# Kernel optimization log

Hardware: AMD Instinct MI355X
Metric: run time of the kernel (lower is better)

Reference implementation:

```python
import jax, jax.numpy as jnp
import numpy as np

N_QUBITS = 13
N_LAYERS = 8
DIM = 2 ** N_QUBITS
CDT = jnp.complex64

_X = jnp.array([[0.0, 1.0], [1.0, 0.0]], dtype=CDT)
_Z = jnp.array([[1.0, 0.0], [0.0, -1.0]], dtype=CDT)
_I2 = jnp.eye(2, dtype=CDT)
_CNOT = jnp.array([[1, 0, 0, 0], [0, 1, 0, 0], [0, 0, 0, 1], [0, 0, 1, 0]], dtype=CDT)


def build_ops():
    """Hardware-efficient ansatz: per layer RX on all qubits, RZ on all qubits, CNOT chain."""
    ops = []
    p = 0
    for _ in range(N_LAYERS):
        for q in range(N_QUBITS):
            ops.append(('RX', (q,), p)); p += 1
        for q in range(N_QUBITS):
            ops.append(('RZ', (q,), p)); p += 1
        for q in range(N_QUBITS - 1):
            ops.append(('CNOT', (q, q + 1), None))
    return ops, p

OPS, N_PARAMS = build_ops()


def _rot(generator, theta):
    # U = cos(theta/2) I - i sin(theta/2) G
    h = theta * 0.5
    return jnp.cos(h).astype(CDT) * _I2 - 1j * jnp.sin(h).astype(CDT) * generator


def _apply_1q(state, U, q):
    st = state.reshape((2,) * N_QUBITS)
    st = jnp.tensordot(U, st, axes=([1], [q]))  # contracted axis moves to front
    return jnp.moveaxis(st, 0, q).reshape(-1)


def _apply_2q(state, U, q0, q1):
    st = state.reshape((2,) * N_QUBITS)
    st = jnp.tensordot(U.reshape(2, 2, 2, 2), st, axes=([2, 3], [q0, q1]))
    return jnp.moveaxis(st, (0, 1), (q0, q1)).reshape(-1)


def _run_circuit(params):
    state = jnp.zeros(DIM, dtype=CDT).at[0].set(1.0)
    for gate, qubits, pidx in OPS:
        if gate == 'RX':
            state = _apply_1q(state, _rot(_X, params[pidx]), qubits[0])
        elif gate == 'RZ':
            state = _apply_1q(state, _rot(_Z, params[pidx]), qubits[0])
        else:  # CNOT
            state = _apply_2q(state, _CNOT, qubits[0], qubits[1])
    return state


def setup_inputs() -> dict:
    key = jax.random.key(0)
    k1, k2 = jax.random.split(key)
    params = jax.random.normal(k1, (N_PARAMS,), dtype=jnp.float32)
    observable = jax.random.normal(k2, (DIM, DIM), dtype=jnp.float32)
    return {"params": params, "observable": observable}


def reference(params, observable) -> jnp.ndarray:
    psi = _run_circuit(params)                      # [2^n] complex64
    obs_psi = observable.astype(CDT) @ psi          # dense observable matvec
    loss = jnp.vdot(psi, obs_psi).real.astype(jnp.float32)  # <psi|O|psi>
    return loss
```

## Files before the change

kernel.cpp:

```cpp
#include <hip/hip_runtime.h>

#define DIM 8192
#define NLAYERS 8
#define SIMT 1024
#define QFB 2048
#define QFT 256
#define ROWS_PER_BLOCK 4

typedef float floatx4 __attribute__((ext_vector_type(4)));
typedef float f2 __attribute__((ext_vector_type(2)));

__device__ __forceinline__ int swz(int i) { return i ^ ((i >> 4) & 15); }

__global__ __launch_bounds__(SIMT) void sim_kernel(const float* __restrict__ params,
                                                   float* __restrict__ outR,
                                                   float* __restrict__ outM) {
    __shared__ f2 buf[2][DIM];
    const int t = threadIdx.x;

    f2 a[8];
#pragma unroll
    for (int l = 0; l < 8; ++l) a[l] = (f2){0.f, 0.f};
    if (t == 0) a[0] = (f2){1.f, 0.f};

    int pp = 0;

    for (int layer = 0; layer < NLAYERS; ++layer) {
        const float* __restrict__ prx = params + layer * 26;
        const float* __restrict__ prz = prx + 13;

        float cb[13], sb[13];
#pragma unroll
        for (int p = 0; p < 13; ++p) __sincosf(0.5f * prx[12 - p], &sb[p], &cb[p]);

#pragma unroll
        for (int k = 0; k < 3; ++k) {
            const f2 c2 = {cb[k], cb[k]};
            const f2 sg = {sb[k], -sb[k]};
#pragma unroll
            for (int l0 = 0; l0 < 8; ++l0) {
                if (!(l0 & (1 << k))) {
                    const int l1 = l0 | (1 << k);
                    const f2 a0 = a[l0], a1 = a[l1];
                    a[l0] = c2 * a0 + __builtin_shufflevector(a1, a1, 1, 0) * sg;
                    a[l1] = c2 * a1 + __builtin_shufflevector(a0, a0, 1, 0) * sg;
                }
            }
        }

        {
            f2* __restrict__ B = buf[pp]; pp ^= 1;
#pragma unroll
            for (int l = 0; l < 8; ++l) B[swz((t << 3) | l)] = a[l];
            __syncthreads();
#pragma unroll
            for (int l = 0; l < 8; ++l)
                a[l] = B[swz((t & 7) | (l << 3) | ((t >> 3) << 6))];
        }

#pragma unroll
        for (int k = 0; k < 3; ++k) {
            const f2 c2 = {cb[3 + k], cb[3 + k]};
            const f2 sg = {sb[3 + k], -sb[3 + k]};
#pragma unroll
            for (int l0 = 0; l0 < 8; ++l0) {
                if (!(l0 & (1 << k))) {
                    const int l1 = l0 | (1 << k);
                    const f2 a0 = a[l0], a1 = a[l1];
                    a[l0] = c2 * a0 + __builtin_shufflevector(a1, a1, 1, 0) * sg;
                    a[l1] = c2 * a1 + __builtin_shufflevector(a0, a0, 1, 0) * sg;
                }
            }
        }

        {
            f2* __restrict__ B = buf[pp]; pp ^= 1;
#pragma unroll
            for (int l = 0; l < 8; ++l)
                B[swz((t & 7) | (l << 3) | ((t >> 3) << 6))] = a[l];
            __syncthreads();
#pragma unroll
            for (int l = 0; l < 8; ++l)
                a[l] = B[swz((t & 63) | (l << 6) | ((t >> 6) << 9))];
        }

#pragma unroll
        for (int k = 0; k < 3; ++k) {
            const f2 c2 = {cb[6 + k], cb[6 + k]};
            const f2 sg = {sb[6 + k], -sb[6 + k]};
#pragma unroll
            for (int l0 = 0; l0 < 8; ++l0) {
                if (!(l0 & (1 << k))) {
                    const int l1 = l0 | (1 << k);
                    const f2 a0 = a[l0], a1 = a[l1];
                    a[l0] = c2 * a0 + __builtin_shufflevector(a1, a1, 1, 0) * sg;
                    a[l1] = c2 * a1 + __builtin_shufflevector(a0, a0, 1, 0) * sg;
                }
            }
        }

        {
            f2* __restrict__ B = buf[pp]; pp ^= 1;
#pragma unroll
            for (int l = 0; l < 8; ++l)
                B[swz((t & 63) | (l << 6) | ((t >> 6) << 9))] = a[l];
            __syncthreads();
#pragma unroll
            for (int l = 0; l < 8; ++l)
                a[l] = B[swz(((t >> 1) & 511) | (l << 9) | ((t & 1) << 12))];
        }

#pragma unroll
        for (int k = 0; k < 3; ++k) {
            const f2 c2 = {cb[9 + k], cb[9 + k]};
            const f2 sg = {sb[9 + k], -sb[9 + k]};
#pragma unroll
            for (int l0 = 0; l0 < 8; ++l0) {
                if (!(l0 & (1 << k))) {
                    const int l1 = l0 | (1 << k);
                    const f2 a0 = a[l0], a1 = a[l1];
                    a[l0] = c2 * a0 + __builtin_shufflevector(a1, a1, 1, 0) * sg;
                    a[l1] = c2 * a1 + __builtin_shufflevector(a0, a0, 1, 0) * sg;
                }
            }
        }

        {
            const f2 c2 = {cb[12], cb[12]};
            const f2 sg = {sb[12], -sb[12]};
#pragma unroll
            for (int l = 0; l < 8; ++l) {
                f2 o;
                o.x = __shfl_xor(a[l].x, 1);
                o.y = __shfl_xor(a[l].y, 1);
                a[l] = c2 * a[l] + __builtin_shufflevector(o, o, 1, 0) * sg;
            }
        }

        float hz[13];
#pragma unroll
        for (int p = 0; p < 13; ++p) hz[p] = 0.5f * prz[12 - p];
        float phiT = 0.f;
#pragma unroll
        for (int p = 0; p < 9; ++p) phiT += (((t >> 1) >> p) & 1) ? hz[p] : -hz[p];
        phiT += (t & 1) ? hz[12] : -hz[12];
#pragma unroll
        for (int l = 0; l < 8; ++l) {
            float phi = phiT;
            phi += (l & 1) ? hz[9]  : -hz[9];
            phi += (l & 2) ? hz[10] : -hz[10];
            phi += (l & 4) ? hz[11] : -hz[11];
            float sp, cp;
            __sincosf(phi, &sp, &cp);
            a[l] = (f2){a[l].x * cp - a[l].y * sp, a[l].x * sp + a[l].y * cp};
        }

        {
            f2* __restrict__ B = buf[pp]; pp ^= 1;
#pragma unroll
            for (int l = 0; l < 8; ++l)
                B[swz(((t >> 1) & 511) | (l << 9) | ((t & 1) << 12))] = a[l];
            __syncthreads();
#pragma unroll
            for (int l = 0; l < 8; ++l) {
                const int c0 = (t << 3) | l;
                a[l] = B[swz(c0 ^ (c0 >> 1))];
            }
        }
    }

    {
        const float4 rv0 = make_float4(a[0].x, a[1].x, a[2].x, a[3].x);
        const float4 rv1 = make_float4(a[4].x, a[5].x, a[6].x, a[7].x);
        const float4 mv0 = make_float4(a[0].y, a[1].y, a[2].y, a[3].y);
        const float4 mv1 = make_float4(a[4].y, a[5].y, a[6].y, a[7].y);
        ((float4*)outR)[2 * t]     = rv0;
        ((float4*)outR)[2 * t + 1] = rv1;
        ((float4*)outM)[2 * t]     = mv0;
        ((float4*)outM)[2 * t + 1] = mv1;
    }
}

__global__ __launch_bounds__(QFT) void quad_kernel(const float* __restrict__ O,
                                                   const float* __restrict__ R,
                                                   const float* __restrict__ M,
                                                   float* __restrict__ partials) {
    const int bi = blockIdx.x;
    const int t  = threadIdx.x;
    const float4* __restrict__ R4 = (const float4*)R;
    const float4* __restrict__ M4 = (const float4*)M;

    float acc = 0.f;
#pragma unroll
    for (int rr = 0; rr < ROWS_PER_BLOCK; ++rr) {
        const int i = bi * ROWS_PER_BLOCK + rr;
        const float ri = R[i];
        const float mi = M[i];
        const floatx4* __restrict__ Or = (const floatx4*)(O + (size_t)i * DIM);
#pragma unroll
        for (int it = 0; it < DIM / 4 / QFT; ++it) {
            const int j4 = t + it * QFT;
            const floatx4 o = __builtin_nontemporal_load(&Or[j4]);
            const float4 rj = R4[j4];
            const float4 mj = M4[j4];
            acc = fmaf(o.x, fmaf(ri, rj.x, mi * mj.x), acc);
            acc = fmaf(o.y, fmaf(ri, rj.y, mi * mj.y), acc);
            acc = fmaf(o.z, fmaf(ri, rj.z, mi * mj.z), acc);
            acc = fmaf(o.w, fmaf(ri, rj.w, mi * mj.w), acc);
        }
    }

#pragma unroll
    for (int off = 32; off > 0; off >>= 1) acc += __shfl_down(acc, off);
    __shared__ float wsum[QFT / 64];
    const int lane = t & 63, w = t >> 6;
    if (lane == 0) wsum[w] = acc;
    __syncthreads();
    if (t == 0) {
        float s = 0.f;
#pragma unroll
        for (int k = 0; k < QFT / 64; ++k) s += wsum[k];
        partials[bi] = s;
    }
}

__global__ __launch_bounds__(256) void reduce_kernel(const float* __restrict__ partials,
                                                     float* __restrict__ out) {
    const int t = threadIdx.x;
    float acc = 0.f;
#pragma unroll
    for (int k = 0; k < QFB / 256; ++k) acc += partials[t + k * 256];
#pragma unroll
    for (int off = 32; off > 0; off >>= 1) acc += __shfl_down(acc, off);
    __shared__ float wsum[4];
    const int lane = t & 63, w = t >> 6;
    if (lane == 0) wsum[w] = acc;
    __syncthreads();
    if (t == 0) out[0] = wsum[0] + wsum[1] + wsum[2] + wsum[3];
}

extern "C" void kernel_launch(void* const* d_in, const int* in_sizes, int n_in,
                              void* d_out, int out_size, void* d_ws, size_t ws_size,
                              hipStream_t stream) {
    const float* params = (const float*)d_in[0];
    const float* O      = (const float*)d_in[1];
    float* out = (float*)d_out;

    float* R        = (float*)d_ws;
    float* M        = R + DIM;
    float* partials = M + DIM;

    sim_kernel<<<1, SIMT, 0, stream>>>(params, R, M);
    quad_kernel<<<QFB, QFT, 0, stream>>>(O, R, M, partials);
    reduce_kernel<<<1, 256, 0, stream>>>(partials, out);
}
```

Measured before the change: 80.65 us.

## Fuse circuit simulation into quadratic-form kernel, recomputing state per block

Removes the separate single-block simulation kernel. Each of 256 blocks now simulates the 13-qubit state redundantly in shared memory and then computes its 32-row slice of psi^T O psi straight from LDS. This drops one kernel launch, the global write and re-read of psi, and the serial dependency between simulation and the large observable stream. The cost is redundant simulation compute in every block and fewer, larger blocks (1024 threads, 128KB LDS), which limits occupancy while the 256MB observable is streamed.

Result: no change. 80.50 us (-0.2%).

```diff
diff --git a/kernel.cpp b/kernel.cpp
--- a/kernel.cpp
+++ b/kernel.cpp
@@ -3,18 +3,17 @@
 #define DIM 8192
 #define NLAYERS 8
 #define SIMT 1024
-#define QFB 2048
-#define QFT 256
-#define ROWS_PER_BLOCK 4
+#define NB 256
+#define QROWS (DIM / NB)
 
 typedef float floatx4 __attribute__((ext_vector_type(4)));
 typedef float f2 __attribute__((ext_vector_type(2)));
 
 __device__ __forceinline__ int swz(int i) { return i ^ ((i >> 4) & 15); }
 
-__global__ __launch_bounds__(SIMT) void sim_kernel(const float* __restrict__ params,
-                                                   float* __restrict__ outR,
-                                                   float* __restrict__ outM) {
+__global__ __launch_bounds__(SIMT) void fused_kernel(const float* __restrict__ params,
+                                                     const float* __restrict__ O,
+                                                     float* __restrict__ partials) {
     __shared__ f2 buf[2][DIM];
     const int t = threadIdx.x;
 
@@ -169,67 +168,54 @@
         }
     }
 
-    {
-        const float4 rv0 = make_float4(a[0].x, a[1].x, a[2].x, a[3].x);
-        const float4 rv1 = make_float4(a[4].x, a[5].x, a[6].x, a[7].x);
-        const float4 mv0 = make_float4(a[0].y, a[1].y, a[2].y, a[3].y);
-        const float4 mv1 = make_float4(a[4].y, a[5].y, a[6].y, a[7].y);
-        ((float4*)outR)[2 * t]     = rv0;
-        ((float4*)outR)[2 * t + 1] = rv1;
-        ((float4*)outM)[2 * t]     = mv0;
-        ((float4*)outM)[2 * t + 1] = mv1;
+    f2* __restrict__ psi = buf[0];
+#pragma unroll
+    for (int l = 0; l < 8; ++l) psi[(t << 3) | l] = a[l];
+    __syncthreads();
+
+    f2 rm[8];
+#pragma unroll
+    for (int c = 0; c < 4; ++c) rm[c]     = psi[4 * t + c];
+#pragma unroll
+    for (int c = 0; c < 4; ++c) rm[4 + c] = psi[4096 + 4 * t + c];
+
+    float acc = 0.f;
+    const int i0 = (int)blockIdx.x * QROWS;
+#pragma unroll 2
+    for (int rr = 0; rr < QROWS; ++rr) {
+        const int i = i0 + rr;
+        const f2 w = psi[i];
+        const floatx4* __restrict__ Or = (const floatx4*)(O + (size_t)i * DIM);
+        const floatx4 o0 = __builtin_nontemporal_load(&Or[t]);
+        const floatx4 o1 = __builtin_nontemporal_load(&Or[t + 1024]);
+        acc = fmaf(o0.x, fmaf(w.x, rm[0].x, w.y * rm[0].y), acc);
+        acc = fmaf(o0.y, fmaf(w.x, rm[1].x, w.y * rm[1].y), acc);
+        acc = fmaf(o0.z, fmaf(w.x, rm[2].x, w.y * rm[2].y), acc);
+        acc = fmaf(o0.w, fmaf(w.x, rm[3].x, w.y * rm[3].y), acc);
+        acc = fmaf(o1.x, fmaf(w.x, rm[4].x, w.y * rm[4].y), acc);
+        acc = fmaf(o1.y, fmaf(w.x, rm[5].x, w.y * rm[5].y), acc);
+        acc = fmaf(o1.z, fmaf(w.x, rm[6].x, w.y * rm[6].y), acc);
+        acc = fmaf(o1.w, fmaf(w.x, rm[7].x, w.y * rm[7].y), acc);
     }
-}
-
-__global__ __launch_bounds__(QFT) void quad_kernel(const float* __restrict__ O,
-                                                   const float* __restrict__ R,
-                                                   const float* __restrict__ M,
-                                                   float* __restrict__ partials) {
-    const int bi = blockIdx.x;
-    const int t  = threadIdx.x;
-    const float4* __restrict__ R4 = (const float4*)R;
-    const float4* __restrict__ M4 = (const float4*)M;
-
-    float acc = 0.f;
-#pragma unroll
-    for (int rr = 0; rr < ROWS_PER_BLOCK; ++rr) {
-        const int i = bi * ROWS_PER_BLOCK + rr;
-        const float ri = R[i];
-        const float mi = M[i];
-        const floatx4* __restrict__ Or = (const floatx4*)(O + (size_t)i * DIM);
-#pragma unroll
-        for (int it = 0; it < DIM / 4 / QFT; ++it) {
-            const int j4 = t + it * QFT;
-            const floatx4 o = __builtin_nontemporal_load(&Or[j4]);
-            const float4 rj = R4[j4];
-            const float4 mj = M4[j4];
-            acc = fmaf(o.x, fmaf(ri, rj.x, mi * mj.x), acc);
-            acc = fmaf(o.y, fmaf(ri, rj.y, mi * mj.y), acc);
-            acc = fmaf(o.z, fmaf(ri, rj.z, mi * mj.z), acc);
-            acc = fmaf(o.w, fmaf(ri, rj.w, mi * mj.w), acc);
-        }
-    }
 
 #pragma unroll
     for (int off = 32; off > 0; off >>= 1) acc += __shfl_down(acc, off);
-    __shared__ float wsum[QFT / 64];
-    const int lane = t & 63, w = t >> 6;
-    if (lane == 0) wsum[w] = acc;
+    __shared__ float wsum[SIMT / 64];
+    const int lane = t & 63, w64 = t >> 6;
+    if (lane == 0) wsum[w64] = acc;
     __syncthreads();
     if (t == 0) {
         float s = 0.f;
 #pragma unroll
-        for (int k = 0; k < QFT / 64; ++k) s += wsum[k];
-        partials[bi] = s;
+        for (int k = 0; k < SIMT / 64; ++k) s += wsum[k];
+        partials[blockIdx.x] = s;
     }
 }
 
 __global__ __launch_bounds__(256) void reduce_kernel(const float* __restrict__ partials,
                                                      float* __restrict__ out) {
     const int t = threadIdx.x;
-    float acc = 0.f;
-#pragma unroll
-    for (int k = 0; k < QFB / 256; ++k) acc += partials[t + k * 256];
+    float acc = partials[t];
 #pragma unroll
     for (int off = 32; off > 0; off >>= 1) acc += __shfl_down(acc, off);
     __shared__ float wsum[4];
@@ -246,11 +232,8 @@
     const float* O      = (const float*)d_in[1];
     float* out = (float*)d_out;
 
-    float* R        = (float*)d_ws;
-    float* M        = R + DIM;
-    float* partials = M + DIM;
-
-    sim_kernel<<<1, SIMT, 0, stream>>>(params, R, M);
-    quad_kernel<<<QFB, QFT, 0, stream>>>(O, R, M, partials);
+    float* partials = (float*)d_ws;
+
+    fused_kernel<<<NB, SIMT, 0, stream>>>(params, O, partials);
     reduce_kernel<<<1, 256, 0, stream>>>(partials, out);
 }
```
